# Kernel tuning notes

Measured on AMD Instinct MI355X. Metric: run time of the kernel, lower is better.

The kernel has to match this reference:

```python
import jax, jax.numpy as jnp
import numpy as np

B, T, IN, H = 4096, 2048, 3, 4

def setup_inputs() -> dict:
    key = jax.random.key(0)
    k1, k2, k3, k4, k5 = jax.random.split(key, 5)
    s_ih = 1.0 / np.sqrt(H)
    return {
        "x": jax.random.normal(k1, (B, T, IN), dtype=jnp.float32),
        # PyTorch LSTM weights, gate order (i, f, g, o), no bias
        "w_ih": jax.random.uniform(k2, (4 * H, IN), dtype=jnp.float32, minval=-s_ih, maxval=s_ih),
        "w_hh": jax.random.uniform(k3, (4 * H, H), dtype=jnp.float32, minval=-s_ih, maxval=s_ih),
        "fc_w": jax.random.uniform(k4, (1, H), dtype=jnp.float32, minval=-0.5, maxval=0.5),
        "fc_b": jax.random.uniform(k5, (1,), dtype=jnp.float32, minval=-0.5, maxval=0.5),
    }

def reference(x, w_ih, w_hh, fc_w, fc_b):
    b = x.shape[0]
    # Precompute input projections for all timesteps in one GEMM: [T, B, 4H]
    xt = jnp.swapaxes(x, 0, 1)                      # [T, B, IN]
    x_proj = jnp.einsum('tbi,gi->tbg', xt, w_ih)    # [T, B, 4H]

    def step(carry, xp):
        h, c = carry
        gates = xp + h @ w_hh.T                     # [B, 4H]
        i, f, g, o = jnp.split(gates, 4, axis=-1)
        i = jax.nn.sigmoid(i)
        f = jax.nn.sigmoid(f)
        g = jnp.tanh(g)
        o = jax.nn.sigmoid(o)
        c = f * c + i * g
        h = o * jnp.tanh(c)
        return (h, c), None

    h0 = jnp.zeros((b, H), dtype=x.dtype)
    c0 = jnp.zeros((b, H), dtype=x.dtype)
    (h_last, _), _ = jax.lax.scan(step, (h0, c0), x_proj)
    # out[:, -1, :] of the LSTM outputs is exactly the final hidden state
    return h_last @ fc_w.T + fc_b                   # [B, 1]
```

## Files before the change

kernel.cpp:

```cpp
#include <hip/hip_runtime.h>


static constexpr int T_STEPS = 2048;
static constexpr int CHUNK   = 16;
static constexpr int NCHUNK  = T_STEPS / CHUNK;

template<int CTRL>
__device__ __forceinline__ float dpp_f(float v) {
    return __int_as_float(__builtin_amdgcn_update_dpp(
        0, __float_as_int(v), CTRL, 0xF, 0xF, false));
}

struct Ctx {
    float wih0, wih1, wih2;
    float W0, W1, W2, W3;
};

template<int J>
__device__ __forceinline__ float comp(const float4& v) {
    if constexpr (J == 0) return v.x;
    else if constexpr (J == 1) return v.y;
    else if constexpr (J == 2) return v.z;
    else return v.w;
}

template<int TT>
__device__ __forceinline__ void projx16(float (&xp)[CHUNK], const float4 (&bf)[12],
                                        const Ctx& k) {
    constexpr int j0 = 3 * TT, j1 = j0 + 1, j2 = j0 + 2;
    float x0 = comp<(j0 & 3)>(bf[j0 >> 2]);
    float x1 = comp<(j1 & 3)>(bf[j1 >> 2]);
    float x2 = comp<(j2 & 3)>(bf[j2 >> 2]);
    xp[TT] = fmaf(x0, k.wih0, fmaf(x1, k.wih1, x2 * k.wih2));
    if constexpr (TT + 1 < CHUNK) projx16<TT + 1>(xp, bf, k);
}

__device__ __forceinline__ void lstm_step(float xp, float& h, float& cp, const Ctx& k) {
    float h1 = dpp_f<0x124>(h);
    float h2 = dpp_f<0x128>(h);
    float h3 = dpp_f<0x12C>(h);
    float a  = fmaf(h,  k.W0, xp);
    a        = fmaf(h1, k.W1, a);
    float bq = h2 * k.W2;
    bq       = fmaf(h3, k.W3, bq);
    float gp = a + bq;
    float e  = __builtin_amdgcn_exp2f(gp);
    float r  = __builtin_amdgcn_rcpf(1.0f + e);
    float ri = dpp_f<0x00>(r);
    float rf = dpp_f<0x55>(r);
    float rg = dpp_f<0xAA>(r);
    float ro = dpp_f<0xFF>(r);
    float t  = fmaf(rg, -5.770780163555854f, 2.885390081777927f);
    float fc = rf * cp;
    float cn = fmaf(ri, t, fc);
    cp = cn;
    float o2 = ro + ro;
    float no = -ro;
    float e2 = __builtin_amdgcn_exp2f(cn);
    float r2 = __builtin_amdgcn_rcpf(1.0f + e2);
    h = fmaf(o2, r2, no);
}

template<int TT>
__device__ __forceinline__ void steps16(const float (&xp)[CHUNK], float& h, float& cp,
                                        const Ctx& k) {
    lstm_step(xp[TT], h, cp, k);
    if constexpr (TT + 1 < CHUNK) steps16<TT + 1>(xp, h, cp, k);
}

__device__ __forceinline__ void loadbf(float4 (&bf)[12], const float4* p) {
    #pragma unroll
    for (int i = 0; i < 12; ++i) bf[i] = p[i];
}

__global__ __launch_bounds__(256, 1) void lstm_kernel(
    const float* __restrict__ x,
    const float* __restrict__ w_ih,
    const float* __restrict__ w_hh,
    const float* __restrict__ fc_w,
    const float* __restrict__ fc_b,
    float* __restrict__ out)
{
    const int tid = threadIdx.x;
    const int l16 = tid & 15;
    const int b   = blockIdx.x * 16 + (tid >> 4);
    const int q   = l16 & 3;
    const int j   = l16 >> 2;

    float t1p = dpp_f<0x124>((float)l16);
    const bool dirB = (t1p == (float)((l16 + 4) & 15));

    const int row = 4 * q + j;
    const float mq = (q == 2) ? -2.885390081777927f : -1.4426950408889634f;

    Ctx k;
    k.wih0 = mq * w_ih[row * 3 + 0];
    k.wih1 = mq * w_ih[row * 3 + 1];
    k.wih2 = mq * w_ih[row * 3 + 2];
    {
        const int u1 = (j + (dirB ? 1 : -1) + 4) & 3;
        const int u2 = (j + (dirB ? 2 : -2) + 4) & 3;
        const int u3 = (j + (dirB ? 3 : -3) + 4) & 3;
        k.W0 = mq * w_hh[row * 4 + j];
        k.W1 = mq * w_hh[row * 4 + u1];
        k.W2 = mq * w_hh[row * 4 + u2];
        k.W3 = mq * w_hh[row * 4 + u3];
    }

    const float4* xb4 = reinterpret_cast<const float4*>(x + (size_t)b * (T_STEPS * 3));

    float4 bfA[12], bfB[12];
    float  xpA[CHUNK], xpB[CHUNK];
    loadbf(bfA, xb4);
    loadbf(bfB, xb4 + 12);
    projx16<0>(xpA, bfA, k);

    float h = 0.f, cp = 0.f;

    for (int it = 0; it < NCHUNK / 2; ++it) {
        const int ca = (2 * it + 2 < NCHUNK) ? 2 * it + 2 : NCHUNK - 1;
        loadbf(bfA, xb4 + ca * 12);
        projx16<0>(xpB, bfB, k);
        steps16<0>(xpA, h, cp, k);

        const int cb = (2 * it + 3 < NCHUNK) ? 2 * it + 3 : NCHUNK - 1;
        loadbf(bfB, xb4 + cb * 12);
        projx16<0>(xpA, bfA, k);
        steps16<0>(xpB, h, cp, k);
    }

    float rr = h * fc_w[j];
    float s1 = rr + dpp_f<0x124>(rr);
    float s2 = s1 + dpp_f<0x128>(s1);
    if (l16 == 0) out[b] = s2 + fc_b[0];
}

extern "C" void kernel_launch(void* const* d_in, const int* in_sizes, int n_in,
                              void* d_out, int out_size, void* d_ws, size_t ws_size,
                              hipStream_t stream) {
    const float* x    = (const float*)d_in[0];
    const float* w_ih = (const float*)d_in[1];
    const float* w_hh = (const float*)d_in[2];
    const float* fc_w = (const float*)d_in[3];
    const float* fc_b = (const float*)d_in[4];
    float* out = (float*)d_out;

    dim3 grid(4096 / 16);
    dim3 block(256);
    hipLaunchKernelGGL(lstm_kernel, grid, block, 0, stream,
                       x, w_ih, w_hh, fc_w, fc_b, out);
}
```

Before: 171.4 us.

## Split hidden-state recurrence so o-gate terms are precomputed off the critical path

Rewrites the LSTM step algebraically so that h = o2*r2 - o is never formed explicitly. The o-gate-dependent products (W*o2 across lanes) and the -0.5*W*o2 + next x-projection sum are computed while the tanh(c) exp/rcp is in flight. The next step then needs only r2 broadcasts and four FMAs, which shortens the serial dependency chain per timestep. In exchange it adds extra DPP shuffles and multiplies per step, and uses more registers for carried state.

```diff
diff --git a/kernel.cpp b/kernel.cpp
--- a/kernel.cpp
+++ b/kernel.cpp
@@ -14,6 +14,12 @@
 struct Ctx {
     float wih0, wih1, wih2;
     float W0, W1, W2, W3;
+    float Wn0, Wn1, Wn2, Wn3;
+};
+
+struct St {
+    float r2, cp, o2;
+    float s, b0, b1, b2, b3;
 };
 
 template<int J>
@@ -35,37 +41,48 @@
     if constexpr (TT + 1 < CHUNK) projx16<TT + 1>(xp, bf, k);
 }
 
-__device__ __forceinline__ void lstm_step(float xp, float& h, float& cp, const Ctx& k) {
-    float h1 = dpp_f<0x124>(h);
-    float h2 = dpp_f<0x128>(h);
-    float h3 = dpp_f<0x12C>(h);
-    float a  = fmaf(h,  k.W0, xp);
-    a        = fmaf(h1, k.W1, a);
-    float bq = h2 * k.W2;
-    bq       = fmaf(h3, k.W3, bq);
-    float gp = a + bq;
-    float e  = __builtin_amdgcn_exp2f(gp);
-    float r  = __builtin_amdgcn_rcpf(1.0f + e);
-    float ri = dpp_f<0x00>(r);
-    float rf = dpp_f<0x55>(r);
-    float rg = dpp_f<0xAA>(r);
-    float ro = dpp_f<0xFF>(r);
-    float t  = fmaf(rg, -5.770780163555854f, 2.885390081777927f);
-    float fc = rf * cp;
-    float cn = fmaf(ri, t, fc);
-    cp = cn;
-    float o2 = ro + ro;
-    float no = -ro;
-    float e2 = __builtin_amdgcn_exp2f(cn);
-    float r2 = __builtin_amdgcn_rcpf(1.0f + e2);
-    h = fmaf(o2, r2, no);
+__device__ __forceinline__ void lstm_step(float xpn, St& S, const Ctx& k) {
+    float r21 = dpp_f<0x124>(S.r2);
+    float r22 = dpp_f<0x128>(S.r2);
+    float r23 = dpp_f<0x12C>(S.r2);
+    float p   = fmaf(S.b0, S.r2, S.s);
+    p         = fmaf(S.b1, r21, p);
+    float q   = S.b2 * r22;
+    q         = fmaf(S.b3, r23, q);
+    float gp  = p + q;
+    float e   = __builtin_amdgcn_exp2f(gp);
+    float r   = __builtin_amdgcn_rcpf(1.0f + e);
+    float rg  = dpp_f<0xAA>(r);
+    float rf  = dpp_f<0x55>(r);
+    float ri  = dpp_f<0x00>(r);
+    float ro  = dpp_f<0xFF>(r);
+    float t   = fmaf(rg, -5.770780163555854f, 2.885390081777927f);
+    float fc  = rf * S.cp;
+    float cn  = fmaf(ri, t, fc);
+    S.cp = cn;
+    float e2  = __builtin_amdgcn_exp2f(cn);
+    float o2  = ro + ro;
+    float o21 = dpp_f<0x124>(o2);
+    float o22 = dpp_f<0x128>(o2);
+    float o23 = dpp_f<0x12C>(o2);
+    S.b0 = k.W0 * o2;
+    S.b1 = k.W1 * o21;
+    S.b2 = k.W2 * o22;
+    S.b3 = k.W3 * o23;
+    float s = fmaf(k.Wn0, o2,  xpn);
+    s       = fmaf(k.Wn1, o21, s);
+    s       = fmaf(k.Wn2, o22, s);
+    s       = fmaf(k.Wn3, o23, s);
+    S.s  = s;
+    S.o2 = o2;
+    S.r2 = __builtin_amdgcn_rcpf(1.0f + e2);
 }
 
 template<int TT>
-__device__ __forceinline__ void steps16(const float (&xp)[CHUNK], float& h, float& cp,
-                                        const Ctx& k) {
-    lstm_step(xp[TT], h, cp, k);
-    if constexpr (TT + 1 < CHUNK) steps16<TT + 1>(xp, h, cp, k);
+__device__ __forceinline__ void steps16(const float (&xp)[CHUNK], float xq,
+                                        St& S, const Ctx& k) {
+    lstm_step((TT + 1 < CHUNK) ? xp[TT + 1] : xq, S, k);
+    if constexpr (TT + 1 < CHUNK) steps16<TT + 1>(xp, xq, S, k);
 }
 
 __device__ __forceinline__ void loadbf(float4 (&bf)[12], const float4* p) {
@@ -106,6 +123,10 @@
         k.W2 = mq * w_hh[row * 4 + u2];
         k.W3 = mq * w_hh[row * 4 + u3];
     }
+    k.Wn0 = -0.5f * k.W0;
+    k.Wn1 = -0.5f * k.W1;
+    k.Wn2 = -0.5f * k.W2;
+    k.Wn3 = -0.5f * k.W3;
 
     const float4* xb4 = reinterpret_cast<const float4*>(x + (size_t)b * (T_STEPS * 3));
 
@@ -115,20 +136,26 @@
     loadbf(bfB, xb4 + 12);
     projx16<0>(xpA, bfA, k);
 
-    float h = 0.f, cp = 0.f;
+    St S;
+    S.cp = 0.f;
+    S.r2 = 0.5f;
+    S.o2 = 0.f;
+    S.b0 = S.b1 = S.b2 = S.b3 = 0.f;
+    S.s  = xpA[0];
 
     for (int it = 0; it < NCHUNK / 2; ++it) {
         const int ca = (2 * it + 2 < NCHUNK) ? 2 * it + 2 : NCHUNK - 1;
         loadbf(bfA, xb4 + ca * 12);
         projx16<0>(xpB, bfB, k);
-        steps16<0>(xpA, h, cp, k);
+        steps16<0>(xpA, xpB[0], S, k);
 
         const int cb = (2 * it + 3 < NCHUNK) ? 2 * it + 3 : NCHUNK - 1;
         loadbf(bfB, xb4 + cb * 12);
         projx16<0>(xpA, bfA, k);
-        steps16<0>(xpB, h, cp, k);
+        steps16<0>(xpB, xpA[0], S, k);
     }
 
+    float h  = S.o2 * (S.r2 - 0.5f);
     float rr = h * fc_w[j];
     float s1 = rr + dpp_f<0x124>(rr);
     float s2 = s1 + dpp_f<0x128>(s1);
```

New measurement: 198.8 us. 1.16x slower.
